# Kernel optimization log

Hardware: AMD Instinct MI355X
Metric: run time of the kernel (lower is better)

Reference implementation:

```python
import jax, jax.numpy as jnp
import numpy as np

DIM, HEADS = 512, 8
HD = DIM // HEADS            # 64
WS = (8, 8)                  # window_size
DS = (2, 2)                  # dilated_size
TW = (WS[0] * DS[0], WS[1] * DS[1])  # total_window_size = (16,16)
SHIFT = (4, 4)


def _rope_tables():
    # Axial 2D RoPE over the (Wh, Ww) window grid: first half of head_dim
    # encodes the h coordinate, second half the w coordinate.
    da = HD // 2
    inv = 1.0 / (10000.0 ** (np.arange(0, da, 2) / da))        # (da/2,)
    ah = np.arange(WS[0])[:, None] * inv                        # (Wh, da/2)
    aw = np.arange(WS[1])[:, None] * inv                        # (Ww, da/2)
    ang = np.concatenate([
        np.broadcast_to(ah[:, None, :], (WS[0], WS[1], da // 2)),
        np.broadcast_to(aw[None, :, :], (WS[0], WS[1], da // 2)),
    ], axis=-1)                                                 # (Wh, Ww, HD/2)
    return jnp.asarray(np.cos(ang), jnp.float32), jnp.asarray(np.sin(ang), jnp.float32)


def _apply_rope(x, cos, sin):
    # x: (M, Wh, Ww, HD); rotate consecutive pairs
    xr = x.reshape(*x.shape[:-1], HD // 2, 2)
    x1, x2 = xr[..., 0], xr[..., 1]
    out = jnp.stack([x1 * cos - x2 * sin, x1 * sin + x2 * cos], axis=-1)
    return out.reshape(x.shape)


def _attn_mask(H, W):
    # Faithful to create_mask (incl. the quirky w_slices where slice(-8,0) is
    # empty and slice(0,None) overwrites the whole row band).
    img = np.zeros((H, W), np.float32)
    cnt = 0
    for hs in (slice(0, -WS[0]), slice(-WS[0], -SHIFT[0]), slice(-SHIFT[0], None)):
        for wsl in (slice(0, -WS[1]), slice(-WS[1], 0), slice(0, None)):
            img[hs, wsl] = cnt
            cnt += 1
    th, tw = TW
    m = img.reshape(H // th, th, W // tw, tw).transpose(0, 2, 1, 3).reshape(-1, th, tw)
    nW = m.shape[0]
    dh, dw = DS
    m = m.reshape(nW, th // dh, dh, tw // dw, dw).transpose(0, 1, 3, 2, 4)
    m = m.reshape(nW, -1, dh * dw).transpose(0, 2, 1).reshape(nW * dh * dw, -1)  # (nW*4, 64)
    diff = m[:, None, :] - m[:, :, None]
    return jnp.asarray(np.where(diff != 0, -1e9, 0.0).astype(np.float32))


def _windows(t):
    # roll -> total-window partition -> dilated partition (Swin-style)
    B, H, W, C = t.shape
    t = jnp.roll(t, (-SHIFT[0], -SHIFT[1]), axis=(1, 2))
    th, tw = TW
    t = t.reshape(B, H // th, th, W // tw, tw, C).transpose(0, 1, 3, 2, 4, 5).reshape(-1, th, tw, C)
    Bw = t.shape[0]                                            # B * nW
    dh, dw = DS
    t = t.reshape(Bw, th // dh, dh, tw // dw, dw, C).transpose(0, 1, 3, 2, 4, 5)
    t = t.reshape(Bw, -1, dh * dw, C).transpose(0, 2, 1, 3).reshape(Bw * dh * dw, -1, C)
    return t, Bw                                               # (Bw*4, 64, C)


def setup_inputs() -> dict:
    key = jax.random.key(0)
    ks = jax.random.split(key, 8)
    B, H, W, C = 4, 128, 128, DIM
    s = 0.02
    return {
        "x": jax.random.normal(ks[0], (B, H, W, C), jnp.float32),
        "cross": jax.random.normal(ks[1], (B, H, W, C), jnp.float32),
        "qv_w": jax.random.normal(ks[2], (C, 2 * C), jnp.float32) * s,
        "qv_b": jnp.zeros((2 * C,), jnp.float32),
        "k_w": jax.random.normal(ks[3], (C, C), jnp.float32) * s,
        "k_b": jnp.zeros((C,), jnp.float32),
        "proj_w": jax.random.normal(ks[4], (C, C), jnp.float32) * s,
        "proj_b": jnp.zeros((C,), jnp.float32),
    }


def reference(x, cross, qv_w, qv_b, k_w, k_b, proj_w, proj_b):
    B, H, W, C = x.shape
    scale = HD ** -0.5
    xw, Bw = _windows(x)
    cw, _ = _windows(cross)
    B_, N, _ = xw.shape                                        # N = 64
    qv = (xw @ qv_w + qv_b).reshape(B_, N, 2, HEADS, HD).transpose(2, 0, 3, 1, 4)
    q, v = qv[0], qv[1]                                        # (B_, h, N, HD)
    k = (cw @ k_w + k_b).reshape(B_, N, HEADS, HD).transpose(0, 2, 1, 3)
    cos, sin = _rope_tables()
    q = _apply_rope(q.reshape(-1, WS[0], WS[1], HD), cos, sin).reshape(B_, HEADS, N, HD)
    k = _apply_rope(k.reshape(-1, WS[0], WS[1], HD), cos, sin).reshape(B_, HEADS, N, HD)
    attn = jnp.einsum('bhnd,bhmd->bhnm', q * scale, k)
    mask = _attn_mask(H, W)                                    # (nW*4, N, N)
    nWd = mask.shape[0]
    attn = attn.reshape(B_ // nWd, nWd, HEADS, N, N) + mask[None, :, None]
    attn = jax.nn.softmax(attn, axis=-1).reshape(B_, HEADS, N, N)
    out = jnp.einsum('bhnm,bhmd->bhnd', attn, v).transpose(0, 2, 1, 3).reshape(B_, N, C)
    # reverse dilation, then reverse total windows, then un-roll
    dh, dw = DS
    th, tw = TW
    out = out.reshape(Bw, dh * dw, N, C).transpose(0, 2, 1, 3).reshape(-1, dh * dw, C)
    out = out.reshape(Bw, th // dh, tw // dw, dh, dw, C).transpose(0, 1, 3, 2, 4, 5).reshape(Bw, th, tw, C)
    out = out.reshape(B, H // th, W // tw, th, tw, C).transpose(0, 1, 3, 2, 4, 5).reshape(B, H, W, C)
    out = jnp.roll(out, (SHIFT[0], SHIFT[1]), axis=(1, 2))
    return out @ proj_w + proj_b
```

## Files before the change

kernel.cpp:

```cpp
#include <hip/hip_runtime.h>


typedef float v4f __attribute__((ext_vector_type(4)));
typedef short short8 __attribute__((ext_vector_type(8)));
typedef unsigned short us4 __attribute__((ext_vector_type(4)));

#define BM 128
#define BN 128

__device__ __forceinline__ unsigned short f2bf(float f) {
  unsigned int u = __builtin_bit_cast(unsigned int, f);
  u += 0x7fffu + ((u >> 16) & 1u);
  return (unsigned short)(u >> 16);
}

__device__ __forceinline__ int tok2pix(int tok) {
  int g = tok >> 6, n = tok & 63;
  int b = g >> 8, rem = g & 255;
  int d = rem & 3, bw = rem >> 2;
  int wh = bw >> 3, ww = bw & 7;
  int ph = n >> 3, pw = n & 7;
  int ii = (wh * 16 + 2 * ph + (d >> 1) + 4) & 127;
  int jj = (ww * 16 + 2 * pw + (d & 1) + 4) & 127;
  return (b * 128 + ii) * 128 + jj;
}

__global__ __launch_bounds__(256) void prep_kernel(
    const float* __restrict__ qv_w, const float* __restrict__ k_w,
    const float* __restrict__ proj_w,
    unsigned short* __restrict__ qv_wt, unsigned short* __restrict__ k_wt,
    unsigned short* __restrict__ proj_wt,
    float* __restrict__ rope_cos, float* __restrict__ rope_sin) {
  int tid = blockIdx.x * 256 + threadIdx.x;
  if (tid < 524288) {
    int c = tid >> 9, k = tid & 511;
    qv_wt[tid] = f2bf(qv_w[k * 1024 + c]);
  } else if (tid < 786432) {
    int t = tid - 524288;
    int c = t >> 9, k = t & 511;
    k_wt[t] = f2bf(k_w[k * 512 + c]);
  } else if (tid < 1048576) {
    int t = tid - 786432;
    int c = t >> 9, k = t & 511;
    proj_wt[t] = f2bf(proj_w[k * 512 + c]);
  } else if (tid < 1048576 + 2048) {
    int t = tid - 1048576;
    int pos = t >> 5, tt = t & 31;
    int ph = pos >> 3, pw = pos & 7;
    float e = (float)(tt & 15) * (1.0f / 16.0f);
    float inv = powf(10000.0f, -e);
    float ang = (float)(tt < 16 ? ph : pw) * inv;
    rope_cos[t] = cosf(ang);
    rope_sin[t] = sinf(ang);
  }
}

template <int MODE>
__global__ __launch_bounds__(256) void gemm_kernel(
    const void* __restrict__ Ap, const unsigned short* __restrict__ Wt,
    const float* __restrict__ bias, void* __restrict__ out0,
    void* __restrict__ out1, const float* __restrict__ rope_cos,
    const float* __restrict__ rope_sin) {
  __shared__ __attribute__((aligned(16))) unsigned short As[4096];
  __shared__ __attribute__((aligned(16))) unsigned short Bs[4096];
  int tid = threadIdx.x;

  constexpr int NBN = (MODE == 0) ? 8 : 4;
  constexpr int NWG = 512 * NBN;
  constexpr int CPX = NWG / 8;
  int lin = blockIdx.x;
  int wgid = (lin & 7) * CPX + (lin >> 3);
  int bm = wgid / NBN;
  int bn = wgid % NBN;

  int lane = tid & 63, wid = tid >> 6;
  int wm = (wid & 1) * 64, wn = (wid >> 1) * 64;
  int l15 = lane & 15, quad = lane >> 4;

  int srow = tid >> 1;
  int shalf = tid & 1;
  int tokA = bm * BM + srow;
  const float* aptr_f = nullptr;
  const unsigned short* aptr_h = nullptr;
  if (MODE == 2) aptr_h = (const unsigned short*)Ap + (size_t)tokA * 512;
  else           aptr_f = (const float*)Ap + (size_t)tok2pix(tokA) * 512;
  const unsigned short* bptr = Wt + (size_t)(bn * BN + srow) * 512;

  v4f acc[4][4];
#pragma unroll
  for (int i = 0; i < 4; i++)
#pragma unroll
    for (int j = 0; j < 4; j++) acc[i][j] = (v4f){0.f, 0.f, 0.f, 0.f};

  for (int k0 = 0; k0 < 512; k0 += 32) {
    if (MODE == 2) {
#pragma unroll
      for (int s = 0; s < 2; s++) {
        int h = shalf * 2 + s;
        short8 v = *(const short8*)(aptr_h + k0 + shalf * 16 + s * 8);
        *(short8*)(As + ((h * 128 + (srow ^ h)) << 3)) = v;
      }
    } else {
#pragma unroll
      for (int s = 0; s < 2; s++) {
        int h = shalf * 2 + s;
        v4f t0 = *(const v4f*)(aptr_f + k0 + shalf * 16 + s * 8);
        v4f t1 = *(const v4f*)(aptr_f + k0 + shalf * 16 + s * 8 + 4);
        short8 w;
        w[0] = (short)f2bf(t0[0]); w[1] = (short)f2bf(t0[1]);
        w[2] = (short)f2bf(t0[2]); w[3] = (short)f2bf(t0[3]);
        w[4] = (short)f2bf(t1[0]); w[5] = (short)f2bf(t1[1]);
        w[6] = (short)f2bf(t1[2]); w[7] = (short)f2bf(t1[3]);
        *(short8*)(As + ((h * 128 + (srow ^ h)) << 3)) = w;
      }
    }
#pragma unroll
    for (int s = 0; s < 2; s++) {
      int h = shalf * 2 + s;
      short8 v = *(const short8*)(bptr + k0 + shalf * 16 + s * 8);
      *(short8*)(Bs + ((h * 128 + (srow ^ h)) << 3)) = v;
    }
    __syncthreads();
    short8 af[4], bfr[4];
#pragma unroll
    for (int i = 0; i < 4; i++)
      af[i] = *(const short8*)(As + ((quad * 128 + ((wm + i * 16 + l15) ^ quad)) << 3));
#pragma unroll
    for (int j = 0; j < 4; j++)
      bfr[j] = *(const short8*)(Bs + ((quad * 128 + ((wn + j * 16 + l15) ^ quad)) << 3));
#pragma unroll
    for (int i = 0; i < 4; i++)
#pragma unroll
      for (int j = 0; j < 4; j++)
        acc[i][j] = __builtin_amdgcn_mfma_f32_16x16x32_bf16(af[i], bfr[j], acc[i][j], 0, 0, 0);
    __syncthreads();
  }

#pragma unroll
  for (int j = 0; j < 4; j++) {
    int col = bn * BN + wn + j * 16 + l15;
    float bv = bias[col];
    int which = col >> 9;
    int h = (col >> 6) & 7;
    int hd = col & 63;
#pragma unroll
    for (int i = 0; i < 4; i++) {
      int tok0 = bm * BM + wm + i * 16 + quad * 4;
      if (MODE == 0 && which == 1) {
        int g = tok0 >> 6, n0 = tok0 & 63;
        us4 wv;
#pragma unroll
        for (int r = 0; r < 4; r++) wv[r] = f2bf(acc[i][j][r] + bv);
        *(us4*)((unsigned short*)out1 + ((((g * 8 + h) * 64 + hd) << 6) + n0)) = wv;
      } else if (MODE == 2) {
#pragma unroll
        for (int r = 0; r < 4; r++)
          ((float*)out0)[(size_t)tok2pix(tok0 + r) * 512 + col] = acc[i][j][r] + bv;
      } else {
#pragma unroll
        for (int r = 0; r < 4; r++) {
          int tok = tok0 + r;
          int g = tok >> 6, n = tok & 63;
          float val = acc[i][j][r] + bv;
          float part = __shfl_xor(val, 1);
          int ti = (n << 5) + (hd >> 1);
          float c = rope_cos[ti], s = rope_sin[ti];
          float o = (hd & 1) ? (part * s + val * c) : (val * c - part * s);
          if (MODE == 0) o *= 0.125f;
          ((unsigned short*)out0)[(((g * 8 + h) * 64 + n) << 6) + hd] = f2bf(o);
        }
      }
    }
  }
}

__global__ __launch_bounds__(256) void attn_kernel(
    const unsigned short* __restrict__ Qbuf, const unsigned short* __restrict__ Kbuf,
    const unsigned short* __restrict__ Vbuf, unsigned short* __restrict__ Obuf) {
  __shared__ __attribute__((aligned(16))) unsigned short Ps[4096];
  int bid = blockIdx.x;
  int g = bid >> 3, h = bid & 7;
  int tid = threadIdx.x;
  int lane = tid & 63, w = tid >> 6;
  int l15 = lane & 15, quad = lane >> 4;
  size_t base = ((size_t)(g * 8 + h)) << 12;
  const unsigned short* Q = Qbuf + base;
  const unsigned short* K = Kbuf + base;
  const unsigned short* Vt = Vbuf + base;

  v4f s[4];
#pragma unroll
  for (int j = 0; j < 4; j++) s[j] = (v4f){0.f, 0.f, 0.f, 0.f};
#pragma unroll
  for (int ki = 0; ki < 2; ki++) {
    short8 aq = *(const short8*)(Q + (w * 16 + l15) * 64 + ki * 32 + quad * 8);
#pragma unroll
    for (int j = 0; j < 4; j++) {
      short8 bk = *(const short8*)(K + (j * 16 + l15) * 64 + ki * 32 + quad * 8);
      s[j] = __builtin_amdgcn_mfma_f32_16x16x32_bf16(aq, bk, s[j], 0, 0, 0);
    }
  }

  int rem = g & 255;
  bool masked_win = ((rem >> 5) == 7);
  float p[4][4];
#pragma unroll
  for (int j = 0; j < 4; j++) {
    int m = j * 16 + l15;
    int pm = m >> 3;
    int gm = (int)(pm >= 4) + (int)(pm >= 6);
#pragma unroll
    for (int r = 0; r < 4; r++) {
      int row = w * 16 + quad * 4 + r;
      int pq = row >> 3;
      int gq = (int)(pq >= 4) + (int)(pq >= 6);
      float v = s[j][r];
      if (masked_win && gm != gq) v = -1e9f;
      p[j][r] = v;
    }
  }
#pragma unroll
  for (int r = 0; r < 4; r++) {
    float mx = fmaxf(fmaxf(p[0][r], p[1][r]), fmaxf(p[2][r], p[3][r]));
    mx = fmaxf(mx, __shfl_xor(mx, 1));
    mx = fmaxf(mx, __shfl_xor(mx, 2));
    mx = fmaxf(mx, __shfl_xor(mx, 4));
    mx = fmaxf(mx, __shfl_xor(mx, 8));
    float sum = 0.f;
#pragma unroll
    for (int j = 0; j < 4; j++) { p[j][r] = __expf(p[j][r] - mx); sum += p[j][r]; }
    sum += __shfl_xor(sum, 1);
    sum += __shfl_xor(sum, 2);
    sum += __shfl_xor(sum, 4);
    sum += __shfl_xor(sum, 8);
    float inv = 1.0f / sum;
    int row = w * 16 + quad * 4 + r;
#pragma unroll
    for (int j = 0; j < 4; j++) {
      int m = j * 16 + l15;
      int h8 = m >> 3;
      Ps[((h8 * 64 + (row ^ h8)) << 3) + (m & 7)] = f2bf(p[j][r] * inv);
    }
  }
  __syncthreads();

  v4f o[4];
#pragma unroll
  for (int j = 0; j < 4; j++) o[j] = (v4f){0.f, 0.f, 0.f, 0.f};
#pragma unroll
  for (int ki = 0; ki < 2; ki++) {
    int h8 = ki * 4 + quad;
    short8 ap = *(const short8*)(Ps + ((h8 * 64 + ((w * 16 + l15) ^ h8)) << 3));
#pragma unroll
    for (int j = 0; j < 4; j++) {
      short8 bv = *(const short8*)(Vt + (j * 16 + l15) * 64 + ki * 32 + quad * 8);
      o[j] = __builtin_amdgcn_mfma_f32_16x16x32_bf16(ap, bv, o[j], 0, 0, 0);
    }
  }
#pragma unroll
  for (int j = 0; j < 4; j++) {
    int hd = j * 16 + l15;
#pragma unroll
    for (int r = 0; r < 4; r++) {
      int row = w * 16 + quad * 4 + r;
      Obuf[(size_t)(g * 64 + row) * 512 + h * 64 + hd] = f2bf(o[j][r]);
    }
  }
}

extern "C" void kernel_launch(void* const* d_in, const int* in_sizes, int n_in,
                              void* d_out, int out_size, void* d_ws, size_t ws_size,
                              hipStream_t stream) {
  const float* x      = (const float*)d_in[0];
  const float* cross  = (const float*)d_in[1];
  const float* qv_w   = (const float*)d_in[2];
  const float* qv_b   = (const float*)d_in[3];
  const float* k_w    = (const float*)d_in[4];
  const float* k_b    = (const float*)d_in[5];
  const float* proj_w = (const float*)d_in[6];
  const float* proj_b = (const float*)d_in[7];

  char* ws = (char*)d_ws;
  const size_t MB = 1024 * 1024;
  unsigned short* Qbuf = (unsigned short*)(ws);
  unsigned short* Kbuf = (unsigned short*)(ws + 64 * MB);
  unsigned short* Vbuf = (unsigned short*)(ws + 128 * MB);
  unsigned short* Obuf = (unsigned short*)(ws + 192 * MB);
  unsigned short* qv_wt = (unsigned short*)(ws + 256 * MB);
  unsigned short* k_wt = qv_wt + 1024 * 512;
  unsigned short* proj_wt = k_wt + 512 * 512;
  float* rope_cos = (float*)(proj_wt + 512 * 512);
  float* rope_sin = rope_cos + 2048;

  prep_kernel<<<4104, 256, 0, stream>>>(qv_w, k_w, proj_w, qv_wt, k_wt, proj_wt,
                                        rope_cos, rope_sin);
  gemm_kernel<0><<<4096, 256, 0, stream>>>(x, qv_wt, qv_b, Qbuf, Vbuf,
                                           rope_cos, rope_sin);
  gemm_kernel<1><<<2048, 256, 0, stream>>>(cross, k_wt, k_b, Kbuf, nullptr,
                                           rope_cos, rope_sin);
  attn_kernel<<<8192, 256, 0, stream>>>(Qbuf, Kbuf, Vbuf, Obuf);
  gemm_kernel<2><<<2048, 256, 0, stream>>>(Obuf, proj_wt, proj_b, d_out, nullptr,
                                           rope_cos, rope_sin);
}
```

Measured before the change: 792.7 us.

## Pre-convert inputs to bf16 and load GEMM tiles via direct global-to-LDS loads

Adds a standalone kernel that converts x and cross from fp32 to bf16 into a scratch buffer before the projection GEMMs. All three GEMM modes then read bf16 and fill shared memory with global_load_lds 16-byte transfers instead of going through registers. This removes the in-loop fp32-to-bf16 conversion and the VGPR staging of tiles. In exchange it adds two extra full-size passes over memory (fp32 read plus bf16 write) and reuses the Obuf region as scratch.

After: 782.5 us. About the same (-1.3%).

```diff
diff --git a/kernel.cpp b/kernel.cpp
--- a/kernel.cpp
+++ b/kernel.cpp
@@ -12,6 +12,11 @@
   unsigned int u = __builtin_bit_cast(unsigned int, f);
   u += 0x7fffu + ((u >> 16) & 1u);
   return (unsigned short)(u >> 16);
+}
+
+__device__ __forceinline__ void gload_lds16(const void* g, void* l) {
+  __builtin_amdgcn_global_load_lds((const __attribute__((address_space(1))) void*)g,
+                                   (__attribute__((address_space(3))) void*)l, 16, 0, 0);
 }
 
 __device__ __forceinline__ int tok2pix(int tok) {
@@ -55,9 +60,25 @@
   }
 }
 
+__global__ __launch_bounds__(256) void convert_kernel(
+    const float* __restrict__ in, unsigned short* __restrict__ out) {
+  unsigned int stride = gridDim.x * 256u;
+  for (unsigned int i = blockIdx.x * 256u + threadIdx.x; i < 4194304u; i += stride) {
+    size_t e = (size_t)i * 8;
+    v4f t0 = *(const v4f*)(in + e);
+    v4f t1 = *(const v4f*)(in + e + 4);
+    short8 w;
+    w[0] = (short)f2bf(t0[0]); w[1] = (short)f2bf(t0[1]);
+    w[2] = (short)f2bf(t0[2]); w[3] = (short)f2bf(t0[3]);
+    w[4] = (short)f2bf(t1[0]); w[5] = (short)f2bf(t1[1]);
+    w[6] = (short)f2bf(t1[2]); w[7] = (short)f2bf(t1[3]);
+    *(short8*)(out + e) = w;
+  }
+}
+
 template <int MODE>
 __global__ __launch_bounds__(256) void gemm_kernel(
-    const void* __restrict__ Ap, const unsigned short* __restrict__ Wt,
+    const unsigned short* __restrict__ Ap, const unsigned short* __restrict__ Wt,
     const float* __restrict__ bias, void* __restrict__ out0,
     void* __restrict__ out1, const float* __restrict__ rope_cos,
     const float* __restrict__ rope_sin) {
@@ -77,14 +98,21 @@
   int wm = (wid & 1) * 64, wn = (wid >> 1) * 64;
   int l15 = lane & 15, quad = lane >> 4;
 
-  int srow = tid >> 1;
-  int shalf = tid & 1;
-  int tokA = bm * BM + srow;
-  const float* aptr_f = nullptr;
-  const unsigned short* aptr_h = nullptr;
-  if (MODE == 2) aptr_h = (const unsigned short*)Ap + (size_t)tokA * 512;
-  else           aptr_f = (const float*)Ap + (size_t)tok2pix(tokA) * 512;
-  const unsigned short* bptr = Wt + (size_t)(bn * BN + srow) * 512;
+  const unsigned short* pa[2];
+  const unsigned short* pb[2];
+  unsigned short* lA[2];
+  unsigned short* lB[2];
+#pragma unroll
+  for (int i = 0; i < 2; i++) {
+    int c = i * 256 + tid;
+    int h = c >> 7, row = (c & 127) ^ h;
+    int tokA = bm * BM + row;
+    size_t arow = (MODE == 2) ? (size_t)tokA : (size_t)tok2pix(tokA);
+    pa[i] = Ap + arow * 512 + h * 8;
+    pb[i] = Wt + (size_t)(bn * BN + row) * 512 + h * 8;
+    lA[i] = As + (size_t)(i * 256 + wid * 64) * 8;
+    lB[i] = Bs + (size_t)(i * 256 + wid * 64) * 8;
+  }
 
   v4f acc[4][4];
 #pragma unroll
@@ -93,32 +121,10 @@
     for (int j = 0; j < 4; j++) acc[i][j] = (v4f){0.f, 0.f, 0.f, 0.f};
 
   for (int k0 = 0; k0 < 512; k0 += 32) {
-    if (MODE == 2) {
-#pragma unroll
-      for (int s = 0; s < 2; s++) {
-        int h = shalf * 2 + s;
-        short8 v = *(const short8*)(aptr_h + k0 + shalf * 16 + s * 8);
-        *(short8*)(As + ((h * 128 + (srow ^ h)) << 3)) = v;
-      }
-    } else {
-#pragma unroll
-      for (int s = 0; s < 2; s++) {
-        int h = shalf * 2 + s;
-        v4f t0 = *(const v4f*)(aptr_f + k0 + shalf * 16 + s * 8);
-        v4f t1 = *(const v4f*)(aptr_f + k0 + shalf * 16 + s * 8 + 4);
-        short8 w;
-        w[0] = (short)f2bf(t0[0]); w[1] = (short)f2bf(t0[1]);
-        w[2] = (short)f2bf(t0[2]); w[3] = (short)f2bf(t0[3]);
-        w[4] = (short)f2bf(t1[0]); w[5] = (short)f2bf(t1[1]);
-        w[6] = (short)f2bf(t1[2]); w[7] = (short)f2bf(t1[3]);
-        *(short8*)(As + ((h * 128 + (srow ^ h)) << 3)) = w;
-      }
-    }
-#pragma unroll
-    for (int s = 0; s < 2; s++) {
-      int h = shalf * 2 + s;
-      short8 v = *(const short8*)(bptr + k0 + shalf * 16 + s * 8);
-      *(short8*)(Bs + ((h * 128 + (srow ^ h)) << 3)) = v;
+#pragma unroll
+    for (int i = 0; i < 2; i++) {
+      gload_lds16(pa[i] + k0, lA[i]);
+      gload_lds16(pb[i] + k0, lB[i]);
     }
     __syncthreads();
     short8 af[4], bfr[4];
@@ -291,12 +297,15 @@
   unsigned short* proj_wt = k_wt + 512 * 512;
   float* rope_cos = (float*)(proj_wt + 512 * 512);
   float* rope_sin = rope_cos + 2048;
+  unsigned short* cvt = Obuf;
 
   prep_kernel<<<4104, 256, 0, stream>>>(qv_w, k_w, proj_w, qv_wt, k_wt, proj_wt,
                                         rope_cos, rope_sin);
-  gemm_kernel<0><<<4096, 256, 0, stream>>>(x, qv_wt, qv_b, Qbuf, Vbuf,
+  convert_kernel<<<2048, 256, 0, stream>>>(x, cvt);
+  gemm_kernel<0><<<4096, 256, 0, stream>>>(cvt, qv_wt, qv_b, Qbuf, Vbuf,
                                            rope_cos, rope_sin);
-  gemm_kernel<1><<<2048, 256, 0, stream>>>(cross, k_wt, k_b, Kbuf, nullptr,
+  convert_kernel<<<2048, 256, 0, stream>>>(cross, cvt);
+  gemm_kernel<1><<<2048, 256, 0, stream>>>(cvt, k_wt, k_b, Kbuf, nullptr,
                                            rope_cos, rope_sin);
   attn_kernel<<<8192, 256, 0, stream>>>(Qbuf, Kbuf, Vbuf, Obuf);
   gemm_kernel<2><<<2048, 256, 0, stream>>>(Obuf, proj_wt, proj_b, d_out, nullptr,
```
